# Performance work log

Hardware: AMD Instinct MI355X
Metric: run time of the kernel (lower is better)

Reference implementation:

```python
import jax, jax.numpy as jnp
import numpy as np

K = 7                 # kernel_size = inhibition_kernel.shape[3]
PAD = 3               # hardcoded ReflectionPad2d((3,3,3,3))
MEMBRANE_DECAY = 0.99


def setup_inputs() -> dict:
    key = jax.random.key(0)
    k1, k2 = jax.random.split(key)
    B, C, H, W = 16, 16, 64, 64
    # spikes are binary events; sparse-ish activity
    in_spikes = (jax.random.uniform(k1, (B, C, H, W)) < 0.1).astype(jnp.float32)
    # weights: (out_h, out_w, C_in, k, k, C_out), init randn * 1/(k*k)
    weights = jax.random.normal(k2, (H, W, C, K, K, C), dtype=jnp.float32) * (1.0 / (K * K))
    membrane = jnp.ones((B, C, H, W), dtype=jnp.float32)
    return {"in_spikes": in_spikes, "weights": weights, "membrane": membrane}


def reference(in_spikes, weights, membrane):
    B, C, H, W = in_spikes.shape
    # ReflectionPad2d(3) on both spatial dims
    padded = jnp.pad(in_spikes, ((0, 0), (0, 0), (PAD, PAD), (PAD, PAD)), mode="reflect")
    # Extract all kxk patches (stride 1): fixed 49 shifted views -> (B, C, K, K, H, W)
    patches = jnp.stack(
        [padded[:, :, ki:ki + H, kj:kj + W] for ki in range(K) for kj in range(K)],
        axis=2,
    ).reshape(B, C, K, K, H, W)
    # Locally-connected (unshared weights) reduce over (c, ki, kj) per output location (i, j):
    # out[b, m, i, j] = sum_{c,x,y} patches[b, c, x, y, i, j] * weights[i, j, c, x, y, m]
    local = jnp.einsum("bcxyij,ijcxym->bmij", patches, weights)
    # LIF membrane/spike update
    mem = membrane * MEMBRANE_DECAY + local
    spike = (mem > 1).astype(in_spikes.dtype)
    mem = jnp.where(mem > 1, jnp.asarray(1.0, mem.dtype), mem)
    return spike, mem
```

## Files before the change

kernel.cpp:

```cpp
#include <hip/hip_runtime.h>

#define HW 64
#define KTOT 784
#define WPB_BYTES 50176u
#define W_TOTAL_BYTES (4096u * WPB_BYTES)
#define WEND (W_TOTAL_BYTES - 16u)

__device__ __forceinline__ void gl16(const void* g, void* l) {
    __builtin_amdgcn_global_load_lds(
        (const __attribute__((address_space(1))) unsigned int*)g,
        (__attribute__((address_space(3))) unsigned int*)l, 16, 0, 0);
}

__global__ __launch_bounds__(256) void k_transpose(const float* __restrict__ in,
                                                   float* __restrict__ sT) {
    __shared__ float tile[16][66];
    const int c = blockIdx.x >> 6;
    const int h = blockIdx.x & 63;
    const int t = threadIdx.x;
    const int wid = t >> 6, l = t & 63;
#pragma unroll
    for (int p = 0; p < 4; ++p) {
        int b = p * 4 + wid;
        tile[b][l] = in[((b << 4) + c) * 4096 + (h << 6) + l];
    }
    __syncthreads();
    const int base = ((c << 6) | h) << 10;
#pragma unroll
    for (int p = 0; p < 4; ++p) {
        int idx = p * 256 + t;
        sT[base + idx] = tile[idx & 15][idx >> 4];
    }
}

__global__ __launch_bounds__(256) void k_lc(const float* __restrict__ weights,
                                            const float* __restrict__ sT,
                                            float* __restrict__ oc) {
    __shared__ __align__(16) float s_spk[12544];
    __shared__ __align__(16) float s_w[3][2048];
    __shared__ __align__(16) float s_red[1024];

    const int tid = threadIdx.x;
    const int bid = blockIdx.x;
    const int i = bid >> 6, j = bid & 63;
    const int wid = tid >> 6, lane = tid & 63;
    const int m = lane >> 2, bq = lane & 3;

    const char* wbase = (const char*)weights;
    const char* sbase = (const char*)sT;
    const unsigned wblk = (unsigned)bid * WPB_BYTES;

    for (int s = wid; s < 49; s += 4) {
        int k = s * 16 + (lane >> 2);
        int c = (k * 1338) >> 16;
        int xy = k - c * 49;
        int x = (xy * 37) >> 8;
        int y = xy - x * 7;
        int r = i + x - 3; r = r < 0 ? -r : r; r = r > 63 ? 126 - r : r;
        int q = j + y - 3; q = q < 0 ? -q : q; q = q > 63 ? 126 - q : q;
        unsigned off = (unsigned)(((c << 12) | (r << 6) | q) << 6)
                     + (unsigned)((lane & 3) << 4);
        gl16(sbase + off, (char*)s_spk + s * 1024);
    }
#pragma unroll
    for (int nn = 0; nn < 3; ++nn) {
#pragma unroll
        for (int L = 0; L < 2; ++L) {
            unsigned off = wblk + (unsigned)nn * 8192u
                         + (unsigned)((L * 4 + wid) << 10) + (unsigned)(lane << 4);
            off = off > WEND ? WEND : off;
            gl16(wbase + off, (char*)&s_w[nn][0] + ((L * 4 + wid) << 10));
        }
    }
    asm volatile("s_waitcnt vmcnt(0)" ::: "memory");
    __builtin_amdgcn_s_barrier();

    float4 acc = make_float4(0.f, 0.f, 0.f, 0.f);
    int nb = 0;
    for (int n = 0; n < 6; ++n) {
        const float* wb = &s_w[nb][0] + wid * 512 + m;
        const float4* sp = (const float4*)s_spk + (((n << 7) + (wid << 5)) << 2) + bq;
#pragma unroll
        for (int t = 0; t < 32; ++t) {
            float4 s4 = sp[t * 4];
            float w = wb[t * 16];
            acc.x += s4.x * w; acc.y += s4.y * w;
            acc.z += s4.z * w; acc.w += s4.w * w;
        }
        asm volatile("s_waitcnt lgkmcnt(0)" ::: "memory");
        __builtin_amdgcn_s_barrier();
        {
            const int nc = n + 3;
#pragma unroll
            for (int L = 0; L < 2; ++L) {
                unsigned off;
                if (nc <= 6) {
                    off = wblk + (unsigned)nc * 8192u
                        + (unsigned)((L * 4 + wid) << 10) + (unsigned)(lane << 4);
                    off = off > WEND ? WEND : off;
                } else {
                    off = WEND;
                }
                gl16(wbase + off, (char*)&s_w[nb][0] + ((L * 4 + wid) << 10));
            }
        }
        asm volatile("s_waitcnt vmcnt(4)" ::: "memory");
        __builtin_amdgcn_s_barrier();
        nb = nb + 1; if (nb == 3) nb = 0;
    }
    {
        const float* wb = &s_w[0][0] + wid * 64 + m;
        const float4* sp = (const float4*)s_spk + ((768 + (wid << 2)) << 2) + bq;
#pragma unroll
        for (int t = 0; t < 4; ++t) {
            float4 s4 = sp[t * 4];
            float w = wb[t * 16];
            acc.x += s4.x * w; acc.y += s4.y * w;
            acc.z += s4.z * w; acc.w += s4.w * w;
        }
    }

    __syncthreads();
    float4* scr = (float4*)s_red;
    scr[wid * 64 + lane] = acc;
    __syncthreads();
    const int b = tid >> 4, mm = tid & 15;
    const int lane_src = mm * 4 + (b >> 2);
    const int d = b & 3;
    float sum = 0.f;
#pragma unroll
    for (int p = 0; p < 4; ++p) {
        float4 v = scr[p * 64 + lane_src];
        sum += (d == 0) ? v.x : (d == 1) ? v.y : (d == 2) ? v.z : v.w;
    }
    oc[(size_t)bid * 256 + tid] = sum;
}

__global__ __launch_bounds__(256) void k_lif(const float* __restrict__ oc,
                                             const float* __restrict__ membrane,
                                             float* __restrict__ out) {
    __shared__ float tile[64][65];
    const int tb = blockIdx.x;
    const int ij0 = (tb >> 2) * 64;
    const int bm0 = (tb & 3) * 64;
    const int t = threadIdx.x;
    const int r0 = t >> 6;
    const int cl = t & 63;

#pragma unroll
    for (int p = 0; p < 16; ++p) {
        int ijl = p * 4 + r0;
        tile[ijl][cl] = oc[(size_t)(ij0 + ijl) * 256 + bm0 + cl];
    }
    __syncthreads();
#pragma unroll
    for (int p = 0; p < 16; ++p) {
        int bml = p * 4 + r0;
        int ijl = cl;
        float local = tile[ijl][bml];
        size_t idx = (size_t)(bm0 + bml) * 4096 + (ij0 + ijl);
        float memv = membrane[idx] * 0.99f + local;
        float spk = (memv > 1.0f) ? 1.0f : 0.0f;
        float mo = (memv > 1.0f) ? 1.0f : memv;
        out[idx] = spk;
        out[idx + 1048576] = mo;
    }
}

extern "C" void kernel_launch(void* const* d_in, const int* in_sizes, int n_in,
                              void* d_out, int out_size, void* d_ws, size_t ws_size,
                              hipStream_t stream) {
    const float* spikes = (const float*)d_in[0];
    const float* weights = (const float*)d_in[1];
    const float* membrane = (const float*)d_in[2];
    float* out = (float*)d_out;

    float* sT = (float*)d_ws;
    float* oc = (float*)d_ws + (1 << 20);

    k_transpose<<<1024, 256, 0, stream>>>(spikes, sT);
    k_lc<<<4096, 256, 0, stream>>>(weights, sT, oc);
    k_lif<<<256, 256, 0, stream>>>(oc, membrane, out);
}
```

Measured before the change: 306.0 us.

## Use 4x4 register tile over outputs and batches in locally-connected kernel

Each thread now computes a 4x4 block (4 output channels by 4 batch elements) per k-step, loading one float4 of spikes and one float4 of weights. Previously it did 4 FMAs per float4 plus a scalar load. This raises FMA-per-LDS-load intensity and splits the reduction dimension 16 ways across waves and lanes. The final reduction now sums 16 partials staged in the reused spike buffer, which adds LDS traffic in the epilogue and more accumulator registers.

```diff
diff --git a/kernel.cpp b/kernel.cpp
--- a/kernel.cpp
+++ b/kernel.cpp
@@ -11,6 +11,16 @@
         (const __attribute__((address_space(1))) unsigned int*)g,
         (__attribute__((address_space(3))) unsigned int*)l, 16, 0, 0);
 }
+
+#define FMA16(acc0, acc1, acc2, acc3, wv, sv)                                 \
+    acc0.x += wv.x * sv.x; acc0.y += wv.x * sv.y;                             \
+    acc0.z += wv.x * sv.z; acc0.w += wv.x * sv.w;                             \
+    acc1.x += wv.y * sv.x; acc1.y += wv.y * sv.y;                             \
+    acc1.z += wv.y * sv.z; acc1.w += wv.y * sv.w;                             \
+    acc2.x += wv.z * sv.x; acc2.y += wv.z * sv.y;                             \
+    acc2.z += wv.z * sv.z; acc2.w += wv.z * sv.w;                             \
+    acc3.x += wv.w * sv.x; acc3.y += wv.w * sv.y;                             \
+    acc3.z += wv.w * sv.z; acc3.w += wv.w * sv.w;
 
 __global__ __launch_bounds__(256) void k_transpose(const float* __restrict__ in,
                                                    float* __restrict__ sT) {
@@ -38,13 +48,14 @@
                                             float* __restrict__ oc) {
     __shared__ __align__(16) float s_spk[12544];
     __shared__ __align__(16) float s_w[3][2048];
-    __shared__ __align__(16) float s_red[1024];
 
     const int tid = threadIdx.x;
     const int bid = blockIdx.x;
     const int i = bid >> 6, j = bid & 63;
     const int wid = tid >> 6, lane = tid & 63;
-    const int m = lane >> 2, bq = lane & 3;
+    const int kq = (lane >> 4) & 3;
+    const int mq = (lane >> 2) & 3;
+    const int bq = lane & 3;
 
     const char* wbase = (const char*)weights;
     const char* sbase = (const char*)sT;
@@ -75,17 +86,21 @@
     asm volatile("s_waitcnt vmcnt(0)" ::: "memory");
     __builtin_amdgcn_s_barrier();
 
-    float4 acc = make_float4(0.f, 0.f, 0.f, 0.f);
+    float4 acc0 = make_float4(0.f, 0.f, 0.f, 0.f);
+    float4 acc1 = make_float4(0.f, 0.f, 0.f, 0.f);
+    float4 acc2 = make_float4(0.f, 0.f, 0.f, 0.f);
+    float4 acc3 = make_float4(0.f, 0.f, 0.f, 0.f);
+
+    const int klb = wid * 32 + kq;
     int nb = 0;
     for (int n = 0; n < 6; ++n) {
-        const float* wb = &s_w[nb][0] + wid * 512 + m;
-        const float4* sp = (const float4*)s_spk + (((n << 7) + (wid << 5)) << 2) + bq;
+        const float4* sp = (const float4*)s_spk + (((n << 7) + klb) << 2) + bq;
+        const float4* wp = (const float4*)&s_w[nb][0] + (klb << 2) + mq;
 #pragma unroll
-        for (int t = 0; t < 32; ++t) {
-            float4 s4 = sp[t * 4];
-            float w = wb[t * 16];
-            acc.x += s4.x * w; acc.y += s4.y * w;
-            acc.z += s4.z * w; acc.w += s4.w * w;
+        for (int t = 0; t < 8; ++t) {
+            float4 sv = sp[t * 16];
+            float4 wv = wp[t * 16];
+            FMA16(acc0, acc1, acc2, acc3, wv, sv)
         }
         asm volatile("s_waitcnt lgkmcnt(0)" ::: "memory");
         __builtin_amdgcn_s_barrier();
@@ -109,29 +124,28 @@
         nb = nb + 1; if (nb == 3) nb = 0;
     }
     {
-        const float* wb = &s_w[0][0] + wid * 64 + m;
-        const float4* sp = (const float4*)s_spk + ((768 + (wid << 2)) << 2) + bq;
-#pragma unroll
-        for (int t = 0; t < 4; ++t) {
-            float4 s4 = sp[t * 4];
-            float w = wb[t * 16];
-            acc.x += s4.x * w; acc.y += s4.y * w;
-            acc.z += s4.z * w; acc.w += s4.w * w;
-        }
+        const int klt = wid * 4 + kq;
+        float4 sv = *((const float4*)s_spk + ((768 + klt) << 2) + bq);
+        float4 wv = *((const float4*)&s_w[0][0] + (klt << 2) + mq);
+        FMA16(acc0, acc1, acc2, acc3, wv, sv)
     }
 
     __syncthreads();
-    float4* scr = (float4*)s_red;
-    scr[wid * 64 + lane] = acc;
+    float* scr = s_spk;
+    {
+        const int g = wid * 4 + kq;
+        float4* scw = (float4*)scr;
+        scw[(g * 16 + mq * 4 + 0) * 4 + bq] = acc0;
+        scw[(g * 16 + mq * 4 + 1) * 4 + bq] = acc1;
+        scw[(g * 16 + mq * 4 + 2) * 4 + bq] = acc2;
+        scw[(g * 16 + mq * 4 + 3) * 4 + bq] = acc3;
+    }
     __syncthreads();
     const int b = tid >> 4, mm = tid & 15;
-    const int lane_src = mm * 4 + (b >> 2);
-    const int d = b & 3;
     float sum = 0.f;
 #pragma unroll
-    for (int p = 0; p < 4; ++p) {
-        float4 v = scr[p * 64 + lane_src];
-        sum += (d == 0) ? v.x : (d == 1) ? v.y : (d == 2) ? v.z : v.w;
+    for (int g = 0; g < 16; ++g) {
+        sum += scr[g * 256 + mm * 16 + b];
     }
     oc[(size_t)bid * 256 + tid] = sum;
 }
```

Measured after the change: 302.7 us. No clear change (-1.1%).
